# Kernel optimization log

Measured on AMD Instinct MI355X. Metric: run time of the kernel, lower is better.

Reference implementation:

```python
import jax, jax.numpy as jnp
import numpy as np

N = 30000      # nodes
E = 1000000    # edges
G = 256        # graphs
IN = 3         # in_channels
H = 8          # heads
D = 16         # per-head dim
HID = 128      # hidden_dim = H*D
L = 3          # num_layers
KP = 17        # num_keypoints
KPE = 16       # kp_emb_dim
NEG = 0.2      # GATv2 leaky_relu negative slope
EPS = 1e-5     # BatchNorm eps


def setup_inputs() -> dict:
    key = jax.random.key(0)
    ks = jax.random.split(key, 24)
    x = jax.random.normal(ks[0], (N, IN), jnp.float32)
    edge_index = jax.random.randint(ks[1], (2, E), 0, N, jnp.int32)
    batch = jnp.sort(jax.random.randint(ks[2], (N,), 0, G, jnp.int32))
    s_in = 1.0 / np.sqrt(IN + KPE)
    s_h = 1.0 / np.sqrt(HID)
    return {
        "x": x,
        "edge_index": edge_index,
        "batch": batch,
        "kp_emb": jax.random.normal(ks[3], (KP, KPE), jnp.float32),
        "w_in": jax.random.normal(ks[4], (IN + KPE, HID), jnp.float32) * s_in,
        "b_in": jax.random.normal(ks[5], (HID,), jnp.float32) * 0.01,
        "w_l": jax.random.normal(ks[6], (L, HID, HID), jnp.float32) * s_h,
        "w_r": jax.random.normal(ks[7], (L, HID, HID), jnp.float32) * s_h,
        "att": jax.random.normal(ks[8], (L, H, D), jnp.float32) * (1.0 / np.sqrt(D)),
        "conv_bias": jax.random.normal(ks[9], (L, HID), jnp.float32) * 0.01,
        "bn_gamma": jnp.ones((L, HID), jnp.float32) + 0.1 * jax.random.normal(ks[10], (L, HID), jnp.float32),
        "bn_beta": 0.1 * jax.random.normal(ks[11], (L, HID), jnp.float32),
        "bn_mean": 0.1 * jax.random.normal(ks[12], (L, HID), jnp.float32),
        "bn_var": 0.5 + jax.random.uniform(ks[13], (L, HID), jnp.float32),
        "w1": jax.random.normal(ks[14], (HID, 2 * HID), jnp.float32) * s_h,
        "b1": jnp.zeros((2 * HID,), jnp.float32),
        "w2": jax.random.normal(ks[15], (2 * HID, HID), jnp.float32) * (1.0 / np.sqrt(2 * HID)),
        "b2": jnp.zeros((HID,), jnp.float32),
        "w3": jax.random.normal(ks[16], (HID, 2), jnp.float32) * s_h,
        "b3": jnp.zeros((2,), jnp.float32),
    }


def reference(x, edge_index, batch, kp_emb, w_in, b_in, w_l, w_r, att, conv_bias,
              bn_gamma, bn_beta, bn_mean, bn_var, w1, b1, w2, b2, w3, b3):
    n = x.shape[0]
    # keypoint id embedding concat + input projection
    kp_ids = jnp.arange(n) % KP
    h = jnp.concatenate([x, kp_emb[kp_ids]], axis=-1) @ w_in + b_in  # [N, HID]
    # GATv2Conv adds self loops by default
    loops = jnp.arange(n, dtype=edge_index.dtype)
    src = jnp.concatenate([edge_index[0], loops])  # message sources (j)
    dst = jnp.concatenate([edge_index[1], loops])  # message targets (i)
    for l in range(L):
        xl = (h @ w_l[l]).reshape(n, H, D)  # source transform (lin_l)
        xr = (h @ w_r[l]).reshape(n, H, D)  # target transform (lin_r)
        z = xl[src] + xr[dst]                              # [Et, H, D]
        score = jnp.einsum('ehd,hd->eh', jax.nn.leaky_relu(z, NEG), att[l])
        # segment softmax over incoming edges of each dst node
        m = jax.ops.segment_max(score, dst, num_segments=n)
        ex = jnp.exp(score - m[dst])
        denom = jax.ops.segment_sum(ex, dst, num_segments=n)
        alpha = ex / denom[dst]                            # [Et, H]
        msg = xl[src] * alpha[..., None]                   # [Et, H, D]
        out = jax.ops.segment_sum(msg, dst, num_segments=n).reshape(n, HID) + conv_bias[l]
        out = jax.nn.relu(out)
        # BatchNorm1d (eval mode: running stats)
        out = (out - bn_mean[l]) * (bn_gamma[l] / jnp.sqrt(bn_var[l] + EPS)) + bn_beta[l]
        h = h + out  # residual (dropout = identity in eval)
    # global mean pool per graph
    sums = jax.ops.segment_sum(h, batch, num_segments=G)
    cnt = jax.ops.segment_sum(jnp.ones((n, 1), h.dtype), batch, num_segments=G)
    g = sums / jnp.maximum(cnt, 1.0)
    # classifier MLP
    g = jax.nn.elu(g @ w1 + b1)
    g = jax.nn.elu(g @ w2 + b2)
    return g @ w3 + b3  # [G, 2]
```

## Files before the change

kernel.cpp:

```cpp
#include <hip/hip_runtime.h>
#include <hip/hip_bf16.h>

#define N_NODES 30000
#define N_EDGES 1000000
#define N_GRAPHS 256
#define HEADS 8
#define DHEAD 16
#define HIDDEN 128
#define LAYERS 3
#define KPN 17
#define KPE 16
#define NEG_SLOPE 0.2f
#define BN_EPS 1e-5f
#define ET (N_EDGES + N_NODES)
#define NBIN 235
#define BINW 128
#define BINCAP 6144
#define CHUNK 4096

typedef __attribute__((ext_vector_type(8))) short bf16x8;
typedef __attribute__((ext_vector_type(4))) float f32x4;

__device__ __forceinline__ unsigned bf16_rne(float f) {
    unsigned u = __float_as_uint(f);
    return (u + 0x7fffu + ((u >> 16) & 1u)) >> 16;
}

__global__ __launch_bounds__(256) void k_bin(const int* __restrict__ ei,
                                             int* __restrict__ bcnt,
                                             unsigned* __restrict__ bdata) {
    __shared__ int lcnt[NBIN];
    __shared__ int lbase[NBIN];
    int base = blockIdx.x * CHUNK;
    int n = N_EDGES - base; if (n > CHUNK) n = CHUNK;
    for (int i = threadIdx.x; i < NBIN; i += 256) lcnt[i] = 0;
    __syncthreads();
    for (int t = threadIdx.x; t < n; t += 256) {
        int d = ei[N_EDGES + base + t];
        atomicAdd(&lcnt[d >> 7], 1);
    }
    __syncthreads();
    for (int i = threadIdx.x; i < NBIN; i += 256) {
        int c = lcnt[i];
        lbase[i] = c ? atomicAdd(&bcnt[i], c) : 0;
        lcnt[i] = 0;
    }
    __syncthreads();
    for (int t = threadIdx.x; t < n; t += 256) {
        int s = ei[base + t];
        int d = ei[N_EDGES + base + t];
        int b = d >> 7;
        int pos = lbase[b] + atomicAdd(&lcnt[b], 1);
        bdata[(size_t)b * BINCAP + pos] = (unsigned)s | ((unsigned)(d & 127) << 15);
    }
}

__global__ __launch_bounds__(256) void k_bscan(const int* __restrict__ bcnt,
                                               int* __restrict__ bbase,
                                               int* __restrict__ ptr) {
    __shared__ int v[256];
    int t = threadIdx.x;
    int c = 0;
    if (t < NBIN) {
        int nodes = N_NODES - t * BINW; if (nodes > BINW) nodes = BINW;
        c = bcnt[t] + nodes;
    }
    v[t] = c;
    __syncthreads();
    for (int off = 1; off < 256; off <<= 1) {
        int x = (t >= off) ? v[t - off] : 0;
        __syncthreads();
        v[t] += x;
        __syncthreads();
    }
    if (t < NBIN) bbase[t] = v[t] - c;
    if (t == 0) ptr[N_NODES] = ET;
}

__global__ __launch_bounds__(256) void k_place2(const int* __restrict__ bcnt,
                                                const unsigned* __restrict__ bdata,
                                                const int* __restrict__ bbase,
                                                int* __restrict__ ptr,
                                                unsigned short* __restrict__ csr_src) {
    __shared__ int hist[BINW];
    __shared__ int pre[BINW];
    __shared__ int nodestart[BINW];
    __shared__ int lofs[BINW];
    int b = blockIdx.x;
    int tid = threadIdx.x;
    int nNodes = N_NODES - b * BINW; if (nNodes > BINW) nNodes = BINW;
    int n = bcnt[b];
    if (tid < BINW) hist[tid] = (tid < nNodes) ? 1 : 0;
    __syncthreads();
    for (int t = tid; t < n; t += 256)
        atomicAdd(&hist[(bdata[(size_t)b * BINCAP + t] >> 15) & 127], 1);
    __syncthreads();
    if (tid < BINW) pre[tid] = hist[tid];
    __syncthreads();
    for (int off = 1; off < BINW; off <<= 1) {
        int x = (tid >= off && tid < BINW) ? pre[tid - off] : 0;
        __syncthreads();
        if (tid < BINW) pre[tid] += x;
        __syncthreads();
    }
    if (tid < BINW) {
        int ns = bbase[b] + pre[tid] - hist[tid];
        nodestart[tid] = ns;
        if (tid < nNodes) {
            int node = b * BINW + tid;
            ptr[node] = ns;
            csr_src[ns] = (unsigned short)node;
        }
        lofs[tid] = 1;
    }
    __syncthreads();
    for (int t = tid; t < n; t += 256) {
        unsigned e = bdata[(size_t)b * BINCAP + t];
        int dl = (e >> 15) & 127;
        int pos = nodestart[dl] + atomicAdd(&lofs[dl], 1);
        csr_src[pos] = (unsigned short)(e & 0x7fffu);
    }
}

__global__ void k_gptr(const int* __restrict__ batch, int* __restrict__ gptr) {
    int g = blockIdx.x * 256 + threadIdx.x;
    if (g > N_GRAPHS) return;
    if (g == N_GRAPHS) { gptr[g] = N_NODES; return; }
    int lo = 0, hi = N_NODES;
    while (lo < hi) {
        int mid = (lo + hi) >> 1;
        if (batch[mid] < g) lo = mid + 1; else hi = mid;
    }
    gptr[g] = lo;
}

__global__ void k_wconv(const float* __restrict__ w_l, const float* __restrict__ w_r,
                        unsigned short* __restrict__ wT) {
    int t = blockIdx.x * 256 + threadIdx.x;
    if (t >= LAYERS * 256 * 128) return;
    int l = t / (256 * 128);
    int rem = t - l * 256 * 128;
    int c = rem >> 7;
    int k = rem & 127;
    float v = (c < 128) ? w_l[(size_t)l * 16384 + k * 128 + c]
                        : w_r[(size_t)l * 16384 + k * 128 + (c - 128)];
    wT[t] = (unsigned short)bf16_rne(v);
}

__global__ void k_inproj(const float* __restrict__ x, const float* __restrict__ kp_emb,
                         const float* __restrict__ w_in, const float* __restrict__ b_in,
                         float* __restrict__ h, unsigned short* __restrict__ hb) {
    int t = blockIdx.x * 256 + threadIdx.x;
    if (t >= N_NODES * HIDDEN) return;
    int c = t & 127, i = t >> 7;
    float acc = b_in[c];
    const float* xi = x + i * 3;
    acc += xi[0] * w_in[0 * 128 + c];
    acc += xi[1] * w_in[1 * 128 + c];
    acc += xi[2] * w_in[2 * 128 + c];
    const float* kp = kp_emb + (i % KPN) * KPE;
#pragma unroll
    for (int k = 0; k < KPE; ++k) acc += kp[k] * w_in[(3 + k) * 128 + c];
    h[t] = acc;
    hb[t] = (unsigned short)bf16_rne(acc);
}

__global__ __launch_bounds__(256) void k_gemm(const unsigned short* __restrict__ hb,
                                              const unsigned short* __restrict__ wT,
                                              unsigned short* __restrict__ xlb,
                                              unsigned short* __restrict__ xrb) {
    int wave = threadIdx.x >> 6;
    int lane = threadIdx.x & 63;
    int brow = blockIdx.x * 32;
    int lr = lane & 15;
    int lk = lane >> 4;
    int ar0 = brow + lr;
    int ar1 = brow + 16 + lr;
    int ar0c = ar0 < N_NODES ? ar0 : N_NODES - 1;
    int ar1c = ar1 < N_NODES ? ar1 : N_NODES - 1;
    int c0 = wave * 64 + lr;

    const unsigned short* ha0 = hb + (size_t)ar0c * 128 + lk * 8;
    const unsigned short* ha1 = hb + (size_t)ar1c * 128 + lk * 8;
    const unsigned short* wb  = wT + (size_t)c0 * 128 + lk * 8;

    f32x4 acc[2][4];
#pragma unroll
    for (int m = 0; m < 2; ++m)
#pragma unroll
        for (int n = 0; n < 4; ++n) acc[m][n] = (f32x4){0.f, 0.f, 0.f, 0.f};

#pragma unroll
    for (int ks = 0; ks < 4; ++ks) {
        bf16x8 a0 = *(const bf16x8*)(ha0 + ks * 32);
        bf16x8 a1 = *(const bf16x8*)(ha1 + ks * 32);
#pragma unroll
        for (int nt = 0; nt < 4; ++nt) {
            bf16x8 b = *(const bf16x8*)(wb + nt * 16 * 128 + ks * 32);
            acc[0][nt] = __builtin_amdgcn_mfma_f32_16x16x32_bf16(a0, b, acc[0][nt], 0, 0, 0);
            acc[1][nt] = __builtin_amdgcn_mfma_f32_16x16x32_bf16(a1, b, acc[1][nt], 0, 0, 0);
        }
    }

    int drow0 = brow + lk * 4;
#pragma unroll
    for (int mt = 0; mt < 2; ++mt) {
#pragma unroll
        for (int nt = 0; nt < 4; ++nt) {
            int col = c0 + nt * 16;
#pragma unroll
            for (int j = 0; j < 4; ++j) {
                int grow = drow0 + mt * 16 + j;
                if (grow >= N_NODES) continue;
                unsigned short bv = (unsigned short)bf16_rne(acc[mt][nt][j]);
                if (col < 128) xlb[(size_t)grow * 128 + col] = bv;
                else           xrb[(size_t)grow * 128 + (col - 128)] = bv;
            }
        }
    }
}

__global__ __launch_bounds__(256) void k_gat(const unsigned* __restrict__ xlb,
                                             const unsigned* __restrict__ xrb,
                                             const int* __restrict__ ptr,
                                             const unsigned short* __restrict__ csr_src,
                                             const float* __restrict__ att_l,
                                             const float* __restrict__ bias_l,
                                             const float* __restrict__ gamma_l,
                                             const float* __restrict__ beta_l,
                                             const float* __restrict__ mean_l,
                                             const float* __restrict__ var_l,
                                             float* __restrict__ h,
                                             unsigned short* __restrict__ hb) {
    int wid = (blockIdx.x * 256 + threadIdx.x) >> 6;
    int lane = threadIdx.x & 63;
    if (wid >= N_NODES) return;
    int i = wid;
    int grp = lane >> 5;
    int l32 = lane & 31;
    int d0 = 4 * l32;

    uint2 xw = *(const uint2*)(xrb + ((size_t)i << 6) + (l32 << 1));
    float xr0 = __uint_as_float(xw.x << 16);
    float xr1 = __uint_as_float(xw.x & 0xffff0000u);
    float xr2 = __uint_as_float(xw.y << 16);
    float xr3 = __uint_as_float(xw.y & 0xffff0000u);
    const float L2E = 1.44269504089f;
    float4 av = *(const float4*)(att_l + d0);
    av.x *= L2E; av.y *= L2E; av.z *= L2E; av.w *= L2E;
    int e0 = ptr[i], e1 = ptr[i + 1];

    float denom = 0.f, acc0 = 0.f, acc1 = 0.f, acc2 = 0.f, acc3 = 0.f;

#define LDP(KP, WREG, VREG) { \
    int eo = 2 * (KP) + grp; \
    int sr = __shfl(sv, eo); \
    VREG = eo < cnt; \
    int rw = VREG ? sr : 0; \
    WREG = *(const uint2*)(xlb + ((size_t)rw << 6) + (l32 << 1)); \
}
#define PROCP(WREG, VREG) { \
    float v0 = __uint_as_float(WREG.x << 16); \
    float v1 = __uint_as_float(WREG.x & 0xffff0000u); \
    float v2 = __uint_as_float(WREG.y << 16); \
    float v3 = __uint_as_float(WREG.y & 0xffff0000u); \
    float z0 = v0 + xr0, z1 = v1 + xr1, z2 = v2 + xr2, z3 = v3 + xr3; \
    z0 = fmaxf(z0, NEG_SLOPE * z0); \
    z1 = fmaxf(z1, NEG_SLOPE * z1); \
    z2 = fmaxf(z2, NEG_SLOPE * z2); \
    z3 = fmaxf(z3, NEG_SLOPE * z3); \
    float p = z0 * av.x + z1 * av.y + z2 * av.z + z3 * av.w; \
    p += __shfl_xor(p, 1); \
    p += __shfl_xor(p, 2); \
    float ex = VREG ? exp2f(p) : 0.f; \
    denom += ex; \
    acc0 += ex * v0; acc1 += ex * v1; acc2 += ex * v2; acc3 += ex * v3; \
}

    for (int base = e0; base < e1; base += 64) {
        int idx = base + lane;
        int sv = (idx < e1) ? (int)csr_src[idx] : 0;
        int cnt = e1 - base; if (cnt > 64) cnt = 64;
        int np = (cnt + 1) >> 1;

        uint2 w0, w1; bool b0 = false, b1 = false;
        LDP(0, w0, b0);
        if (1 < np) LDP(1, w1, b1);
        int k = 0;
        for (; k + 2 < np; k += 2) {
            uint2 n0, n1; bool c0v, c1v;
            LDP(k + 2, n0, c0v);
            LDP(k + 3, n1, c1v);
            PROCP(w0, b0); PROCP(w1, b1);
            w0 = n0; b0 = c0v; w1 = n1; b1 = c1v;
        }
        PROCP(w0, b0);
        if (k + 1 < np) PROCP(w1, b1);
    }
#undef LDP
#undef PROCP

    denom += __shfl_xor(denom, 32);
    acc0 += __shfl_xor(acc0, 32);
    acc1 += __shfl_xor(acc1, 32);
    acc2 += __shfl_xor(acc2, 32);
    acc3 += __shfl_xor(acc3, 32);

    if (grp == 0) {
        float inv = 1.f / denom;
        float4 bia = *(const float4*)(bias_l + d0);
        float4 gam = *(const float4*)(gamma_l + d0);
        float4 bet = *(const float4*)(beta_l + d0);
        float4 mea = *(const float4*)(mean_l + d0);
        float4 var = *(const float4*)(var_l + d0);
        float o0 = fmaxf(acc0 * inv + bia.x, 0.f);
        float o1 = fmaxf(acc1 * inv + bia.y, 0.f);
        float o2 = fmaxf(acc2 * inv + bia.z, 0.f);
        float o3 = fmaxf(acc3 * inv + bia.w, 0.f);
        o0 = (o0 - mea.x) * (gam.x * rsqrtf(var.x + BN_EPS)) + bet.x;
        o1 = (o1 - mea.y) * (gam.y * rsqrtf(var.y + BN_EPS)) + bet.y;
        o2 = (o2 - mea.z) * (gam.z * rsqrtf(var.z + BN_EPS)) + bet.z;
        o3 = (o3 - mea.w) * (gam.w * rsqrtf(var.w + BN_EPS)) + bet.w;
        float4 hv = *(const float4*)(h + (size_t)i * 128 + d0);
        hv.x += o0; hv.y += o1; hv.z += o2; hv.w += o3;
        *(float4*)(h + (size_t)i * 128 + d0) = hv;
        unsigned pk0 = bf16_rne(hv.x) | (bf16_rne(hv.y) << 16);
        unsigned pk1 = bf16_rne(hv.z) | (bf16_rne(hv.w) << 16);
        uint2 pk; pk.x = pk0; pk.y = pk1;
        *(uint2*)(hb + (size_t)i * 128 + d0) = pk;
    }
}

__global__ __launch_bounds__(256) void k_pool_seg(const float* __restrict__ h,
                                                  const int* __restrict__ gptr,
                                                  float* __restrict__ pool) {
    __shared__ float red[256];
    int b = blockIdx.x;
    int c = threadIdx.x & 127, half = threadIdx.x >> 7;
    int lo = gptr[b], hi = gptr[b + 1];
    float s = 0.f;
    for (int i = lo + half; i < hi; i += 2) s += h[(size_t)i * 128 + c];
    red[threadIdx.x] = s;
    __syncthreads();
    if (half == 0) pool[b * 128 + c] = red[c] + red[c + 128];
}

__global__ __launch_bounds__(256) void k_mlp(const float* __restrict__ pool,
                                             const int* __restrict__ gptr,
                                             const float* __restrict__ w1, const float* __restrict__ b1,
                                             const float* __restrict__ w2, const float* __restrict__ b2,
                                             const float* __restrict__ w3, const float* __restrict__ b3,
                                             float* __restrict__ out) {
    __shared__ float g[128], t1[256], t2[128];
    int b = blockIdx.x, t = threadIdx.x;
    float cnt = fmaxf((float)(gptr[b + 1] - gptr[b]), 1.0f);
    if (t < 128) g[t] = pool[b * 128 + t] / cnt;
    __syncthreads();
    {
        float acc = b1[t];
        for (int k = 0; k < 128; ++k) acc += g[k] * w1[k * 256 + t];
        t1[t] = acc > 0.f ? acc : expm1f(acc);
    }
    __syncthreads();
    if (t < 128) {
        float acc = b2[t];
        for (int k = 0; k < 256; ++k) acc += t1[k] * w2[k * 128 + t];
        t2[t] = acc > 0.f ? acc : expm1f(acc);
    }
    __syncthreads();
    if (t < 2) {
        float acc = b3[t];
        for (int k = 0; k < 128; ++k) acc += t2[k] * w3[k * 2 + t];
        out[b * 2 + t] = acc;
    }
}

extern "C" void kernel_launch(void* const* d_in, const int* in_sizes, int n_in,
                              void* d_out, int out_size, void* d_ws, size_t ws_size,
                              hipStream_t stream) {
    const float* x        = (const float*)d_in[0];
    const int*   ei       = (const int*)d_in[1];
    const int*   batch    = (const int*)d_in[2];
    const float* kp_emb   = (const float*)d_in[3];
    const float* w_in     = (const float*)d_in[4];
    const float* b_in     = (const float*)d_in[5];
    const float* w_l      = (const float*)d_in[6];
    const float* w_r      = (const float*)d_in[7];
    const float* att      = (const float*)d_in[8];
    const float* conv_b   = (const float*)d_in[9];
    const float* bn_gamma = (const float*)d_in[10];
    const float* bn_beta  = (const float*)d_in[11];
    const float* bn_mean  = (const float*)d_in[12];
    const float* bn_var   = (const float*)d_in[13];
    const float* w1 = (const float*)d_in[14];
    const float* b1 = (const float*)d_in[15];
    const float* w2 = (const float*)d_in[16];
    const float* b2 = (const float*)d_in[17];
    const float* w3 = (const float*)d_in[18];
    const float* b3 = (const float*)d_in[19];
    float* out = (float*)d_out;

    char* ws = (char*)d_ws;
    const size_t OFF_H    = 0;
    const size_t OFF_HB   = OFF_H    + 15360000;
    const size_t OFF_XL   = OFF_HB   + 7680000;
    const size_t OFF_XR   = OFF_XL   + 7680000;
    const size_t OFF_WT   = OFF_XR   + 7680000;
    const size_t OFF_PTR  = OFF_WT   + 196608;
    const size_t OFF_BCNT = OFF_PTR  + 120320;
    const size_t OFF_BBAS = OFF_BCNT + 1024;
    const size_t OFF_SRC  = OFF_BBAS + 1024;
    const size_t OFF_POOL = OFF_SRC  + 2060032;
    const size_t OFF_GPTR = OFF_POOL + 131072;

    float*          h      = (float*)(ws + OFF_H);
    unsigned short* hb     = (unsigned short*)(ws + OFF_HB);
    unsigned short* xlb    = (unsigned short*)(ws + OFF_XL);
    unsigned short* xrb    = (unsigned short*)(ws + OFF_XR);
    unsigned*       bdata  = (unsigned*)(ws + OFF_XR);
    unsigned short* wT     = (unsigned short*)(ws + OFF_WT);
    int*            ptr    = (int*)(ws + OFF_PTR);
    int*            bcnt   = (int*)(ws + OFF_BCNT);
    int*            bbase  = (int*)(ws + OFF_BBAS);
    unsigned short* csrsrc = (unsigned short*)(ws + OFF_SRC);
    float*          pool   = (float*)(ws + OFF_POOL);
    int*            gptr   = (int*)(ws + OFF_GPTR);

    hipMemsetAsync(bcnt, 0, NBIN * 4, stream);
    k_bin<<<(N_EDGES + CHUNK - 1) / CHUNK, 256, 0, stream>>>(ei, bcnt, bdata);
    k_bscan<<<1, 256, 0, stream>>>(bcnt, bbase, ptr);
    k_place2<<<NBIN, 256, 0, stream>>>(bcnt, bdata, bbase, ptr, csrsrc);
    k_gptr<<<2, 256, 0, stream>>>(batch, gptr);
    k_wconv<<<(LAYERS * 256 * 128 + 255) / 256, 256, 0, stream>>>(w_l, w_r, wT);

    k_inproj<<<(N_NODES * 128 + 255) / 256, 256, 0, stream>>>(x, kp_emb, w_in, b_in, h, hb);

    for (int l = 0; l < LAYERS; ++l) {
        k_gemm<<<(N_NODES + 31) / 32, 256, 0, stream>>>(hb, wT + (size_t)l * 256 * 128, xlb, xrb);
        k_gat<<<(N_NODES + 3) / 4, 256, 0, stream>>>(
            (const unsigned*)xlb, (const unsigned*)xrb, ptr, csrsrc,
            att + (size_t)l * 128, conv_b + (size_t)l * 128,
            bn_gamma + (size_t)l * 128, bn_beta + (size_t)l * 128,
            bn_mean + (size_t)l * 128, bn_var + (size_t)l * 128, h, hb);
    }

    k_pool_seg<<<N_GRAPHS, 256, 0, stream>>>(h, gptr, pool);
    k_mlp<<<N_GRAPHS, 256, 0, stream>>>(pool, gptr, w1, b1, w2, b2, w3, b3, out);
}
```

Measured before the change: 284.8 us.

## Fuse preprocessing kernels, input projection into GEMM, pool into MLP, split CSR by source half

Several changes land together. Graph-pointer search, weight conversion and edge binning now run in one launch, the bin-base scan moves into the placement kernel, and the input projection is fused into the first-layer GEMM through shared memory. Pooling is merged into the classifier MLP, and GEMM outputs are staged in LDS so they can be written with vectorized stores. The CSR source lists are also ordered per destination so low-index sources come before high-index ones, which may improve gather locality in the attention kernel. Together these cut launch count and intermediate global traffic, at the cost of every placement block redoing the scan and the fused GEMM recomputing the projection inline.

```diff
diff --git a/kernel.cpp b/kernel.cpp
--- a/kernel.cpp
+++ b/kernel.cpp
@@ -17,6 +17,9 @@
 #define BINW 128
 #define BINCAP 6144
 #define CHUNK 4096
+#define NB_EDGE 245
+#define NB_WCONV 384
+#define SRC_HALF 15000
 
 typedef __attribute__((ext_vector_type(8))) short bf16x8;
 typedef __attribute__((ext_vector_type(4))) float f32x4;
@@ -28,161 +31,189 @@
 
 __global__ __launch_bounds__(256) void k_bin(const int* __restrict__ ei,
                                              int* __restrict__ bcnt,
-                                             unsigned* __restrict__ bdata) {
-    __shared__ int lcnt[NBIN];
-    __shared__ int lbase[NBIN];
-    int base = blockIdx.x * CHUNK;
-    int n = N_EDGES - base; if (n > CHUNK) n = CHUNK;
-    for (int i = threadIdx.x; i < NBIN; i += 256) lcnt[i] = 0;
-    __syncthreads();
-    for (int t = threadIdx.x; t < n; t += 256) {
-        int d = ei[N_EDGES + base + t];
-        atomicAdd(&lcnt[d >> 7], 1);
-    }
-    __syncthreads();
-    for (int i = threadIdx.x; i < NBIN; i += 256) {
-        int c = lcnt[i];
-        lbase[i] = c ? atomicAdd(&bcnt[i], c) : 0;
-        lcnt[i] = 0;
-    }
-    __syncthreads();
-    for (int t = threadIdx.x; t < n; t += 256) {
-        int s = ei[base + t];
-        int d = ei[N_EDGES + base + t];
-        int b = d >> 7;
-        int pos = lbase[b] + atomicAdd(&lcnt[b], 1);
-        bdata[(size_t)b * BINCAP + pos] = (unsigned)s | ((unsigned)(d & 127) << 15);
-    }
-}
-
-__global__ __launch_bounds__(256) void k_bscan(const int* __restrict__ bcnt,
-                                               int* __restrict__ bbase,
-                                               int* __restrict__ ptr) {
-    __shared__ int v[256];
-    int t = threadIdx.x;
-    int c = 0;
-    if (t < NBIN) {
-        int nodes = N_NODES - t * BINW; if (nodes > BINW) nodes = BINW;
-        c = bcnt[t] + nodes;
-    }
-    v[t] = c;
-    __syncthreads();
-    for (int off = 1; off < 256; off <<= 1) {
-        int x = (t >= off) ? v[t - off] : 0;
-        __syncthreads();
-        v[t] += x;
-        __syncthreads();
-    }
-    if (t < NBIN) bbase[t] = v[t] - c;
-    if (t == 0) ptr[N_NODES] = ET;
+                                             unsigned* __restrict__ bdata,
+                                             const int* __restrict__ batch,
+                                             int* __restrict__ gptr,
+                                             int* __restrict__ ptr,
+                                             const float* __restrict__ w_l,
+                                             const float* __restrict__ w_r,
+                                             unsigned short* __restrict__ wT) {
+    int bid = blockIdx.x;
+    if (bid < NB_EDGE) {
+        __shared__ int lcnt[NBIN];
+        __shared__ int lbase[NBIN];
+        int base = bid * CHUNK;
+        int n = N_EDGES - base; if (n > CHUNK) n = CHUNK;
+        for (int i = threadIdx.x; i < NBIN; i += 256) lcnt[i] = 0;
+        __syncthreads();
+        for (int t = threadIdx.x; t < n; t += 256) {
+            int d = ei[N_EDGES + base + t];
+            atomicAdd(&lcnt[d >> 7], 1);
+        }
+        __syncthreads();
+        for (int i = threadIdx.x; i < NBIN; i += 256) {
+            int c = lcnt[i];
+            lbase[i] = c ? atomicAdd(&bcnt[i], c) : 0;
+            lcnt[i] = 0;
+        }
+        __syncthreads();
+        for (int t = threadIdx.x; t < n; t += 256) {
+            int s = ei[base + t];
+            int d = ei[N_EDGES + base + t];
+            int b = d >> 7;
+            int pos = lbase[b] + atomicAdd(&lcnt[b], 1);
+            bdata[(size_t)b * BINCAP + pos] = (unsigned)s | ((unsigned)(d & 127) << 15);
+        }
+    } else if (bid == NB_EDGE) {
+        for (int g = threadIdx.x; g <= N_GRAPHS; g += 256) {
+            if (g == N_GRAPHS) { gptr[g] = N_NODES; }
+            else {
+                int lo = 0, hi = N_NODES;
+                while (lo < hi) {
+                    int mid = (lo + hi) >> 1;
+                    if (batch[mid] < g) lo = mid + 1; else hi = mid;
+                }
+                gptr[g] = lo;
+            }
+        }
+        if (threadIdx.x == 0) ptr[N_NODES] = ET;
+    } else {
+        int idx = (bid - NB_EDGE - 1) * 256 + threadIdx.x;
+        if (idx < LAYERS * 256 * 128) {
+            int l = idx / (256 * 128);
+            int rem = idx - l * 256 * 128;
+            int c = rem >> 7;
+            int k = rem & 127;
+            float v = (c < 128) ? w_l[(size_t)l * 16384 + k * 128 + c]
+                                : w_r[(size_t)l * 16384 + k * 128 + (c - 128)];
+            wT[idx] = (unsigned short)bf16_rne(v);
+        }
+    }
 }
 
 __global__ __launch_bounds__(256) void k_place2(const int* __restrict__ bcnt,
                                                 const unsigned* __restrict__ bdata,
-                                                const int* __restrict__ bbase,
                                                 int* __restrict__ ptr,
                                                 unsigned short* __restrict__ csr_src) {
-    __shared__ int hist[BINW];
-    __shared__ int pre[BINW];
-    __shared__ int nodestart[BINW];
-    __shared__ int lofs[BINW];
-    int b = blockIdx.x;
-    int tid = threadIdx.x;
+    __shared__ int vsc[256];
+    __shared__ int histL[BINW], histH[BINW];
+    __shared__ int lowS[BINW], highS[BINW];
+    __shared__ int lofsL[BINW], lofsH[BINW];
+    __shared__ int bbase_sh;
+    int b = blockIdx.x, tid = threadIdx.x;
+
+    int c = 0;
+    if (tid < NBIN) {
+        int nodes = N_NODES - tid * BINW; if (nodes > BINW) nodes = BINW;
+        c = bcnt[tid] + nodes;
+    }
+    vsc[tid] = c;
+    __syncthreads();
+    for (int off = 1; off < 256; off <<= 1) {
+        int x = (tid >= off) ? vsc[tid - off] : 0;
+        __syncthreads();
+        vsc[tid] += x;
+        __syncthreads();
+    }
+    if (tid == 0) bbase_sh = (b == 0) ? 0 : vsc[b - 1];
+
     int nNodes = N_NODES - b * BINW; if (nNodes > BINW) nNodes = BINW;
     int n = bcnt[b];
-    if (tid < BINW) hist[tid] = (tid < nNodes) ? 1 : 0;
-    __syncthreads();
-    for (int t = tid; t < n; t += 256)
-        atomicAdd(&hist[(bdata[(size_t)b * BINCAP + t] >> 15) & 127], 1);
-    __syncthreads();
-    if (tid < BINW) pre[tid] = hist[tid];
-    __syncthreads();
-    for (int off = 1; off < BINW; off <<= 1) {
-        int x = (tid >= off && tid < BINW) ? pre[tid - off] : 0;
-        __syncthreads();
-        if (tid < BINW) pre[tid] += x;
-        __syncthreads();
-    }
     if (tid < BINW) {
-        int ns = bbase[b] + pre[tid] - hist[tid];
-        nodestart[tid] = ns;
-        if (tid < nNodes) {
-            int node = b * BINW + tid;
-            ptr[node] = ns;
-            csr_src[ns] = (unsigned short)node;
-        }
-        lofs[tid] = 1;
+        int node = b * BINW + tid;
+        int valid = tid < nNodes;
+        histL[tid] = (valid && node < SRC_HALF) ? 1 : 0;
+        histH[tid] = (valid && node >= SRC_HALF) ? 1 : 0;
     }
     __syncthreads();
     for (int t = tid; t < n; t += 256) {
         unsigned e = bdata[(size_t)b * BINCAP + t];
         int dl = (e >> 15) & 127;
-        int pos = nodestart[dl] + atomicAdd(&lofs[dl], 1);
-        csr_src[pos] = (unsigned short)(e & 0x7fffu);
-    }
-}
-
-__global__ void k_gptr(const int* __restrict__ batch, int* __restrict__ gptr) {
-    int g = blockIdx.x * 256 + threadIdx.x;
-    if (g > N_GRAPHS) return;
-    if (g == N_GRAPHS) { gptr[g] = N_NODES; return; }
-    int lo = 0, hi = N_NODES;
-    while (lo < hi) {
-        int mid = (lo + hi) >> 1;
-        if (batch[mid] < g) lo = mid + 1; else hi = mid;
-    }
-    gptr[g] = lo;
-}
-
-__global__ void k_wconv(const float* __restrict__ w_l, const float* __restrict__ w_r,
-                        unsigned short* __restrict__ wT) {
-    int t = blockIdx.x * 256 + threadIdx.x;
-    if (t >= LAYERS * 256 * 128) return;
-    int l = t / (256 * 128);
-    int rem = t - l * 256 * 128;
-    int c = rem >> 7;
-    int k = rem & 127;
-    float v = (c < 128) ? w_l[(size_t)l * 16384 + k * 128 + c]
-                        : w_r[(size_t)l * 16384 + k * 128 + (c - 128)];
-    wT[t] = (unsigned short)bf16_rne(v);
-}
-
-__global__ void k_inproj(const float* __restrict__ x, const float* __restrict__ kp_emb,
-                         const float* __restrict__ w_in, const float* __restrict__ b_in,
-                         float* __restrict__ h, unsigned short* __restrict__ hb) {
-    int t = blockIdx.x * 256 + threadIdx.x;
-    if (t >= N_NODES * HIDDEN) return;
-    int c = t & 127, i = t >> 7;
-    float acc = b_in[c];
-    const float* xi = x + i * 3;
-    acc += xi[0] * w_in[0 * 128 + c];
-    acc += xi[1] * w_in[1 * 128 + c];
-    acc += xi[2] * w_in[2 * 128 + c];
-    const float* kp = kp_emb + (i % KPN) * KPE;
-#pragma unroll
-    for (int k = 0; k < KPE; ++k) acc += kp[k] * w_in[(3 + k) * 128 + c];
-    h[t] = acc;
-    hb[t] = (unsigned short)bf16_rne(acc);
-}
-
-__global__ __launch_bounds__(256) void k_gemm(const unsigned short* __restrict__ hb,
-                                              const unsigned short* __restrict__ wT,
-                                              unsigned short* __restrict__ xlb,
-                                              unsigned short* __restrict__ xrb) {
-    int wave = threadIdx.x >> 6;
-    int lane = threadIdx.x & 63;
+        if ((e & 0x7fffu) < SRC_HALF) atomicAdd(&histL[dl], 1);
+        else                          atomicAdd(&histH[dl], 1);
+    }
+    __syncthreads();
+    if (tid < BINW) vsc[tid] = histL[tid] + histH[tid];
+    __syncthreads();
+    for (int off = 1; off < BINW; off <<= 1) {
+        int x = (tid >= off && tid < BINW) ? vsc[tid - off] : 0;
+        __syncthreads();
+        if (tid < BINW) vsc[tid] += x;
+        __syncthreads();
+    }
+    if (tid < BINW) {
+        int tot = histL[tid] + histH[tid];
+        int ns = bbase_sh + vsc[tid] - tot;
+        lowS[tid] = ns;
+        highS[tid] = ns + histL[tid];
+        int node = b * BINW + tid;
+        int isLow = node < SRC_HALF;
+        if (tid < nNodes) {
+            ptr[node] = ns;
+            if (isLow) csr_src[ns] = (unsigned short)node;
+            else       csr_src[ns + histL[tid]] = (unsigned short)node;
+        }
+        lofsL[tid] = (tid < nNodes && isLow) ? 1 : 0;
+        lofsH[tid] = (tid < nNodes && !isLow) ? 1 : 0;
+    }
+    __syncthreads();
+    for (int t = tid; t < n; t += 256) {
+        unsigned e = bdata[(size_t)b * BINCAP + t];
+        int dl = (e >> 15) & 127;
+        int s = e & 0x7fffu;
+        int pos = (s < SRC_HALF) ? (lowS[dl] + atomicAdd(&lofsL[dl], 1))
+                                 : (highS[dl] + atomicAdd(&lofsH[dl], 1));
+        csr_src[pos] = (unsigned short)s;
+    }
+}
+
+template<bool FUSED>
+__global__ __launch_bounds__(256) void k_gemmT(const float* __restrict__ x,
+                                               const float* __restrict__ kp_emb,
+                                               const float* __restrict__ w_in,
+                                               const float* __restrict__ b_in,
+                                               float* __restrict__ h,
+                                               const unsigned short* __restrict__ hb,
+                                               const unsigned short* __restrict__ wT,
+                                               unsigned short* __restrict__ xlb,
+                                               unsigned short* __restrict__ xrb) {
+    __shared__ unsigned short hsA[32][136];
+    __shared__ unsigned short st[32][264];
+    int tid = threadIdx.x;
+    int wave = tid >> 6, lane = tid & 63;
     int brow = blockIdx.x * 32;
-    int lr = lane & 15;
-    int lk = lane >> 4;
-    int ar0 = brow + lr;
-    int ar1 = brow + 16 + lr;
-    int ar0c = ar0 < N_NODES ? ar0 : N_NODES - 1;
-    int ar1c = ar1 < N_NODES ? ar1 : N_NODES - 1;
+    int lr = lane & 15, lk = lane >> 4;
+
+    if (FUSED) {
+        int r = tid >> 3, c16 = (tid & 7) * 16;
+        int gr = brow + r;
+        int gc = gr < N_NODES ? gr : 0;
+        float xv0 = x[gc * 3], xv1 = x[gc * 3 + 1], xv2 = x[gc * 3 + 2];
+        const float* kp = kp_emb + (gc % KPN) * KPE;
+        float res[16];
+#pragma unroll
+        for (int q = 0; q < 16; ++q) {
+            int c = c16 + q;
+            float acc = b_in[c] + xv0 * w_in[c] + xv1 * w_in[128 + c] + xv2 * w_in[256 + c];
+#pragma unroll
+            for (int kk = 0; kk < KPE; ++kk) acc += kp[kk] * w_in[(3 + kk) * 128 + c];
+            res[q] = acc;
+        }
+        if (gr < N_NODES) {
+#pragma unroll
+            for (int q = 0; q < 16; q += 4)
+                *(float4*)(h + (size_t)gr * 128 + c16 + q) =
+                    make_float4(res[q], res[q + 1], res[q + 2], res[q + 3]);
+        }
+#pragma unroll
+        for (int q = 0; q < 16; ++q) hsA[r][c16 + q] = (unsigned short)bf16_rne(res[q]);
+        __syncthreads();
+    }
+
+    int ar0c = brow + lr;      if (ar0c >= N_NODES) ar0c = N_NODES - 1;
+    int ar1c = brow + 16 + lr; if (ar1c >= N_NODES) ar1c = N_NODES - 1;
     int c0 = wave * 64 + lr;
-
-    const unsigned short* ha0 = hb + (size_t)ar0c * 128 + lk * 8;
-    const unsigned short* ha1 = hb + (size_t)ar1c * 128 + lk * 8;
-    const unsigned short* wb  = wT + (size_t)c0 * 128 + lk * 8;
+    const unsigned short* wb = wT + (size_t)c0 * 128 + lk * 8;
 
     f32x4 acc[2][4];
 #pragma unroll
@@ -192,8 +223,14 @@
 
 #pragma unroll
     for (int ks = 0; ks < 4; ++ks) {
-        bf16x8 a0 = *(const bf16x8*)(ha0 + ks * 32);
-        bf16x8 a1 = *(const bf16x8*)(ha1 + ks * 32);
+        bf16x8 a0, a1;
+        if (FUSED) {
+            a0 = *(const bf16x8*)&hsA[lr][lk * 8 + ks * 32];
+            a1 = *(const bf16x8*)&hsA[16 + lr][lk * 8 + ks * 32];
+        } else {
+            a0 = *(const bf16x8*)(hb + (size_t)ar0c * 128 + lk * 8 + ks * 32);
+            a1 = *(const bf16x8*)(hb + (size_t)ar1c * 128 + lk * 8 + ks * 32);
+        }
 #pragma unroll
         for (int nt = 0; nt < 4; ++nt) {
             bf16x8 b = *(const bf16x8*)(wb + nt * 16 * 128 + ks * 32);
@@ -202,21 +239,29 @@
         }
     }
 
-    int drow0 = brow + lk * 4;
-#pragma unroll
-    for (int mt = 0; mt < 2; ++mt) {
-#pragma unroll
-        for (int nt = 0; nt < 4; ++nt) {
-            int col = c0 + nt * 16;
-#pragma unroll
-            for (int j = 0; j < 4; ++j) {
-                int grow = drow0 + mt * 16 + j;
-                if (grow >= N_NODES) continue;
-                unsigned short bv = (unsigned short)bf16_rne(acc[mt][nt][j]);
-                if (col < 128) xlb[(size_t)grow * 128 + col] = bv;
-                else           xrb[(size_t)grow * 128 + (col - 128)] = bv;
-            }
-        }
+    int r0 = lk * 4;
+#pragma unroll
+    for (int mt = 0; mt < 2; ++mt)
+#pragma unroll
+        for (int nt = 0; nt < 4; ++nt)
+#pragma unroll
+            for (int j = 0; j < 4; ++j)
+                st[r0 + mt * 16 + j][c0 + nt * 16] = (unsigned short)bf16_rne(acc[mt][nt][j]);
+    __syncthreads();
+
+    int rr = tid >> 3, seg = tid & 7;
+    int grow = brow + rr;
+    if (grow < N_NODES) {
+        uint4 v0 = *(uint4*)&st[rr][seg * 32];
+        uint4 v1 = *(uint4*)&st[rr][seg * 32 + 8];
+        uint4 v2 = *(uint4*)&st[rr][seg * 32 + 16];
+        uint4 v3 = *(uint4*)&st[rr][seg * 32 + 24];
+        unsigned short* dst = (seg < 4) ? (xlb + (size_t)grow * 128 + seg * 32)
+                                        : (xrb + (size_t)grow * 128 + (seg - 4) * 32);
+        *(uint4*)(dst)      = v0;
+        *(uint4*)(dst + 8)  = v1;
+        *(uint4*)(dst + 16) = v2;
+        *(uint4*)(dst + 24) = v3;
     }
 }
 
@@ -331,30 +376,25 @@
     }
 }
 
-__global__ __launch_bounds__(256) void k_pool_seg(const float* __restrict__ h,
-                                                  const int* __restrict__ gptr,
-                                                  float* __restrict__ pool) {
+__global__ __launch_bounds__(256) void k_poolmlp(const float* __restrict__ h,
+                                                 const int* __restrict__ gptr,
+                                                 const float* __restrict__ w1, const float* __restrict__ b1,
+                                                 const float* __restrict__ w2, const float* __restrict__ b2,
+                                                 const float* __restrict__ w3, const float* __restrict__ b3,
+                                                 float* __restrict__ out) {
     __shared__ float red[256];
-    int b = blockIdx.x;
-    int c = threadIdx.x & 127, half = threadIdx.x >> 7;
+    __shared__ float g[128], t1[256], t2[128];
+    int b = blockIdx.x, t = threadIdx.x;
+    int c = t & 127, half = t >> 7;
     int lo = gptr[b], hi = gptr[b + 1];
     float s = 0.f;
     for (int i = lo + half; i < hi; i += 2) s += h[(size_t)i * 128 + c];
-    red[threadIdx.x] = s;
-    __syncthreads();
-    if (half == 0) pool[b * 128 + c] = red[c] + red[c + 128];
-}
-
-__global__ __launch_bounds__(256) void k_mlp(const float* __restrict__ pool,
-                                             const int* __restrict__ gptr,
-                                             const float* __restrict__ w1, const float* __restrict__ b1,
-                                             const float* __restrict__ w2, const float* __restrict__ b2,
-                                             const float* __restrict__ w3, const float* __restrict__ b3,
-                                             float* __restrict__ out) {
-    __shared__ float g[128], t1[256], t2[128];
-    int b = blockIdx.x, t = threadIdx.x;
-    float cnt = fmaxf((float)(gptr[b + 1] - gptr[b]), 1.0f);
-    if (t < 128) g[t] = pool[b * 128 + t] / cnt;
+    red[t] = s;
+    __syncthreads();
+    if (half == 0) {
+        float cntf = fmaxf((float)(hi - lo), 1.0f);
+        g[c] = (red[c] + red[c + 128]) / cntf;
+    }
     __syncthreads();
     {
         float acc = b1[t];
@@ -408,10 +448,8 @@
     const size_t OFF_WT   = OFF_XR   + 7680000;
     const size_t OFF_PTR  = OFF_WT   + 196608;
     const size_t OFF_BCNT = OFF_PTR  + 120320;
-    const size_t OFF_BBAS = OFF_BCNT + 1024;
-    const size_t OFF_SRC  = OFF_BBAS + 1024;
-    const size_t OFF_POOL = OFF_SRC  + 2060032;
-    const size_t OFF_GPTR = OFF_POOL + 131072;
+    const size_t OFF_SRC  = OFF_BCNT + 1024;
+    const size_t OFF_GPTR = OFF_SRC  + 2060032;
 
     float*          h      = (float*)(ws + OFF_H);
     unsigned short* hb     = (unsigned short*)(ws + OFF_HB);
@@ -421,22 +459,22 @@
     unsigned short* wT     = (unsigned short*)(ws + OFF_WT);
     int*            ptr    = (int*)(ws + OFF_PTR);
     int*            bcnt   = (int*)(ws + OFF_BCNT);
-    int*            bbase  = (int*)(ws + OFF_BBAS);
     unsigned short* csrsrc = (unsigned short*)(ws + OFF_SRC);
-    float*          pool   = (float*)(ws + OFF_POOL);
     int*            gptr   = (int*)(ws + OFF_GPTR);
 
     hipMemsetAsync(bcnt, 0, NBIN * 4, stream);
-    k_bin<<<(N_EDGES + CHUNK - 1) / CHUNK, 256, 0, stream>>>(ei, bcnt, bdata);
-    k_bscan<<<1, 256, 0, stream>>>(bcnt, bbase, ptr);
-    k_place2<<<NBIN, 256, 0, stream>>>(bcnt, bdata, bbase, ptr, csrsrc);
-    k_gptr<<<2, 256, 0, stream>>>(batch, gptr);
-    k_wconv<<<(LAYERS * 256 * 128 + 255) / 256, 256, 0, stream>>>(w_l, w_r, wT);
-
-    k_inproj<<<(N_NODES * 128 + 255) / 256, 256, 0, stream>>>(x, kp_emb, w_in, b_in, h, hb);
+    k_bin<<<NB_EDGE + 1 + NB_WCONV, 256, 0, stream>>>(ei, bcnt, bdata, batch, gptr, ptr,
+                                                      w_l, w_r, wT);
+    k_place2<<<NBIN, 256, 0, stream>>>(bcnt, bdata, ptr, csrsrc);
 
     for (int l = 0; l < LAYERS; ++l) {
-        k_gemm<<<(N_NODES + 31) / 32, 256, 0, stream>>>(hb, wT + (size_t)l * 256 * 128, xlb, xrb);
+        const unsigned short* wTl = wT + (size_t)l * 256 * 128;
+        if (l == 0)
+            k_gemmT<true><<<(N_NODES + 31) / 32, 256, 0, stream>>>(
+                x, kp_emb, w_in, b_in, h, hb, wTl, xlb, xrb);
+        else
+            k_gemmT<false><<<(N_NODES + 31) / 32, 256, 0, stream>>>(
+                x, kp_emb, w_in, b_in, h, hb, wTl, xlb, xrb);
         k_gat<<<(N_NODES + 3) / 4, 256, 0, stream>>>(
             (const unsigned*)xlb, (const unsigned*)xrb, ptr, csrsrc,
             att + (size_t)l * 128, conv_b + (size_t)l * 128,
@@ -444,6 +482,5 @@
             bn_mean + (size_t)l * 128, bn_var + (size_t)l * 128, h, hb);
     }
 
-    k_pool_seg<<<N_GRAPHS, 256, 0, stream>>>(h, gptr, pool);
-    k_mlp<<<N_GRAPHS, 256, 0, stream>>>(pool, gptr, w1, b1, w2, b2, w3, b3, out);
-}
+    k_poolmlp<<<N_GRAPHS, 256, 0, stream>>>(h, gptr, w1, b1, w2, b2, w3, b3, out);
+}
```

After: 272.1 us. -4.4%, faster.
